# Kernel tuning notes

Measured on AMD Instinct MI355X. Metric: run time of the kernel, lower is better.

Reference implementation:

```python
import jax, jax.numpy as jnp
import numpy as np


def setup_inputs() -> dict:
    key = jax.random.key(0)
    k1, k2 = jax.random.split(key)
    D = 32            # num_detectors
    IN_S = 64         # input_size per detector
    OUT_S = 64        # output_size per detector
    B = 8192          # batch
    x = jax.random.normal(k1, (B, IN_S * D), dtype=jnp.float32)
    # nn.Linear weight: [out_features, in_features] = [OUT_S*D, IN_S*D]
    W = jax.random.normal(k2, (OUT_S * D, IN_S * D), dtype=jnp.float32) * (1.0 / np.sqrt(IN_S * D))
    return {"x": x, "W": W, "num_detectors": D}


def reference(x, W, num_detectors):
    # Original: y = ((W * block_diag_mask) @ x.T).T
    # The mask zeroes everything except num_detectors diagonal (out_s, in_s)
    # blocks, so this is exactly num_detectors independent linears. We compute
    # only the diagonal blocks (same math; off-diagonal weights contribute 0).
    D = num_detectors
    total_out, total_in = W.shape
    out_s = total_out // D
    in_s = total_in // D
    # extract diagonal blocks -> [D, out_s, in_s]
    Wb = W.reshape(D, out_s, D, in_s)
    d = jnp.arange(D)
    blocks = Wb[d, :, d, :]                      # [D, out_s, in_s]
    xb = x.reshape(x.shape[0], D, in_s)          # [B, D, in_s]
    y = jnp.einsum('bdi,doi->bdo', xb, blocks)   # [B, D, out_s]
    return y.reshape(x.shape[0], D * out_s)
```

## Files before the change

### kernel.cpp

```cpp
#include <hip/hip_runtime.h>

#define NDET    32
#define SEG     64
#define ROWLEN  2048
#define TILE_B  128
#define THREADS 256
#define LSTRIDE 72

typedef __bf16 bf16x8 __attribute__((ext_vector_type(8)));
typedef __bf16 bf16x4 __attribute__((ext_vector_type(4)));
typedef float  f32x4  __attribute__((ext_vector_type(4)));

__device__ __forceinline__ bf16x4 cvt4(f32x4 a) {
  bf16x4 r;
  r[0] = (__bf16)a[0]; r[1] = (__bf16)a[1]; r[2] = (__bf16)a[2]; r[3] = (__bf16)a[3];
  return r;
}

__global__ __launch_bounds__(THREADS) void ensemble_linear_v4(
    const float* __restrict__ x, const float* __restrict__ W,
    float* __restrict__ y) {
  const int d     = blockIdx.y;
  const int b0    = blockIdx.x * TILE_B;
  const int t     = threadIdx.x;
  const int lane  = t & 63;
  const int wid   = t >> 6;
  const int dbase = d * SEG;

  const int rq  = lane >> 4;
  const int c4  = lane & 15;

  __shared__ __bf16 wls[SEG * LSTRIDE];
  __shared__ __bf16 xls[TILE_B * LSTRIDE];

  f32x4 wv[4];
#pragma unroll
  for (int p = 0; p < 4; ++p) {
    const int row = wid * 16 + p * 4 + rq;
    wv[p] = *(const f32x4*)(W + (size_t)(dbase + row) * ROWLEN + dbase + c4 * 4);
  }
  f32x4 xv[8];
#pragma unroll
  for (int p = 0; p < 8; ++p) {
    const int row = wid * 32 + p * 4 + rq;
    xv[p] = *(const f32x4*)(x + (size_t)(b0 + row) * ROWLEN + dbase + c4 * 4);
  }

#pragma unroll
  for (int p = 0; p < 4; ++p) {
    const int row = wid * 16 + p * 4 + rq;
    *(bf16x4*)(&wls[row * LSTRIDE + c4 * 4]) = cvt4(wv[p]);
  }
#pragma unroll
  for (int p = 0; p < 8; ++p) {
    const int row = wid * 32 + p * 4 + rq;
    *(bf16x4*)(&xls[row * LSTRIDE + c4 * 4]) = cvt4(xv[p]);
  }

  __syncthreads();

  const int m16 = lane & 15;
  const int kg  = lane >> 4;

  bf16x8 wfrag[4][2];
#pragma unroll
  for (int g = 0; g < 4; ++g)
#pragma unroll
    for (int kh = 0; kh < 2; ++kh)
      wfrag[g][kh] = *(const bf16x8*)(&wls[(g * 16 + m16) * LSTRIDE + kh * 32 + kg * 8]);

#pragma unroll
  for (int s = 0; s < 2; ++s) {
    const int rbase = wid * 32 + s * 16;
    bf16x8 a0 = *(const bf16x8*)(&xls[(rbase + m16) * LSTRIDE + kg * 8]);
    bf16x8 a1 = *(const bf16x8*)(&xls[(rbase + m16) * LSTRIDE + 32 + kg * 8]);

    float* yp = y + (size_t)(b0 + rbase + m16) * ROWLEN + dbase + kg * 4;
#pragma unroll
    for (int g = 0; g < 4; ++g) {
      f32x4 acc = (f32x4){0.f, 0.f, 0.f, 0.f};
      acc = __builtin_amdgcn_mfma_f32_16x16x32_bf16(wfrag[g][0], a0, acc, 0, 0, 0);
      acc = __builtin_amdgcn_mfma_f32_16x16x32_bf16(wfrag[g][1], a1, acc, 0, 0, 0);
      *(f32x4*)(yp + g * 16) = acc;
    }
  }
}

extern "C" void kernel_launch(void* const* d_in, const int* in_sizes, int n_in,
                              void* d_out, int out_size, void* d_ws, size_t ws_size,
                              hipStream_t stream) {
  const float* x = (const float*)d_in[0];
  const float* W = (const float*)d_in[1];
  float* y = (float*)d_out;
  const int B = in_sizes[0] / ROWLEN;
  dim3 grid(B / TILE_B, NDET);
  ensemble_linear_v4<<<grid, dim3(THREADS), 0, stream>>>(x, W, y);
}
```

Measured before the change: 28.46 us.

## Tile over groups of four detectors with 64-row batch tiles

Each block now handles 64 batch rows across four adjacent detectors instead of 128 rows of one detector. The x loads read 1 KB of contiguous row data per wavefront rather than 256-byte segments, aiming at better coalescing and fewer blocks. The trade-off is that each block loads four weight blocks (64 KB fp32) for only 64 rows, so W traffic per output rises. LDS use and register pressure also grow (16+16 f32x4 staged per thread), which may lower occupancy.

```diff
diff --git a/kernel.cpp b/kernel.cpp
--- a/kernel.cpp
+++ b/kernel.cpp
@@ -3,9 +3,12 @@
 #define NDET    32
 #define SEG     64
 #define ROWLEN  2048
-#define TILE_B  128
+#define DGRP    4
+#define XCOLS   (DGRP * SEG)
+#define TILE_R  64
 #define THREADS 256
-#define LSTRIDE 72
+#define XLSTR   264
+#define WLSTR   72
 
 typedef __bf16 bf16x8 __attribute__((ext_vector_type(8)));
 typedef __bf16 bf16x4 __attribute__((ext_vector_type(4)));
@@ -17,70 +20,65 @@
   return r;
 }
 
-__global__ __launch_bounds__(THREADS) void ensemble_linear_v4(
+__global__ __launch_bounds__(THREADS) void ensemble_linear_v8(
     const float* __restrict__ x, const float* __restrict__ W,
     float* __restrict__ y) {
-  const int d     = blockIdx.y;
-  const int b0    = blockIdx.x * TILE_B;
-  const int t     = threadIdx.x;
-  const int lane  = t & 63;
-  const int wid   = t >> 6;
-  const int dbase = d * SEG;
-
+  const int dg     = blockIdx.y;
+  const int dbase0 = dg * XCOLS;
+  const int r0     = blockIdx.x * TILE_R;
+  const int t      = threadIdx.x;
+  const int lane   = t & 63;
+  const int wid    = t >> 6;
   const int rq  = lane >> 4;
   const int c4  = lane & 15;
+  const int m16 = lane & 15;
+  const int kg  = lane >> 4;
 
-  __shared__ __bf16 wls[SEG * LSTRIDE];
-  __shared__ __bf16 xls[TILE_B * LSTRIDE];
+  __shared__ __bf16 xls[TILE_R * XLSTR];
+  __shared__ __bf16 wls[DGRP * SEG * WLSTR];
 
-  f32x4 wv[4];
+  f32x4 xv[16];
 #pragma unroll
-  for (int p = 0; p < 4; ++p) {
-    const int row = wid * 16 + p * 4 + rq;
-    wv[p] = *(const f32x4*)(W + (size_t)(dbase + row) * ROWLEN + dbase + c4 * 4);
+  for (int p = 0; p < 16; ++p) {
+    const int row = p * 4 + wid;
+    xv[p] = *(const f32x4*)(x + (size_t)(r0 + row) * ROWLEN + dbase0 + lane * 4);
   }
-  f32x4 xv[8];
+
+  f32x4 wv[16];
 #pragma unroll
-  for (int p = 0; p < 8; ++p) {
-    const int row = wid * 32 + p * 4 + rq;
-    xv[p] = *(const f32x4*)(x + (size_t)(b0 + row) * ROWLEN + dbase + c4 * 4);
+  for (int p = 0; p < 16; ++p) {
+    const int o = p * 4 + rq;
+    wv[p] = *(const f32x4*)(W + (size_t)(dbase0 + wid * SEG + o) * ROWLEN
+                              + dbase0 + wid * SEG + c4 * 4);
   }
 
 #pragma unroll
-  for (int p = 0; p < 4; ++p) {
-    const int row = wid * 16 + p * 4 + rq;
-    *(bf16x4*)(&wls[row * LSTRIDE + c4 * 4]) = cvt4(wv[p]);
+  for (int p = 0; p < 16; ++p) {
+    const int row = p * 4 + wid;
+    *(bf16x4*)(&xls[row * XLSTR + lane * 4]) = cvt4(xv[p]);
   }
 #pragma unroll
-  for (int p = 0; p < 8; ++p) {
-    const int row = wid * 32 + p * 4 + rq;
-    *(bf16x4*)(&xls[row * LSTRIDE + c4 * 4]) = cvt4(xv[p]);
+  for (int p = 0; p < 16; ++p) {
+    const int o = p * 4 + rq;
+    *(bf16x4*)(&wls[(wid * SEG + o) * WLSTR + c4 * 4]) = cvt4(wv[p]);
   }
 
   __syncthreads();
 
-  const int m16 = lane & 15;
-  const int kg  = lane >> 4;
+  const int rbase = wid * 16;
+#pragma unroll
+  for (int q = 0; q < DGRP; ++q) {
+    bf16x8 a0 = *(const bf16x8*)(&xls[(rbase + m16) * XLSTR + q * SEG + kg * 8]);
+    bf16x8 a1 = *(const bf16x8*)(&xls[(rbase + m16) * XLSTR + q * SEG + 32 + kg * 8]);
 
-  bf16x8 wfrag[4][2];
-#pragma unroll
-  for (int g = 0; g < 4; ++g)
-#pragma unroll
-    for (int kh = 0; kh < 2; ++kh)
-      wfrag[g][kh] = *(const bf16x8*)(&wls[(g * 16 + m16) * LSTRIDE + kh * 32 + kg * 8]);
-
-#pragma unroll
-  for (int s = 0; s < 2; ++s) {
-    const int rbase = wid * 32 + s * 16;
-    bf16x8 a0 = *(const bf16x8*)(&xls[(rbase + m16) * LSTRIDE + kg * 8]);
-    bf16x8 a1 = *(const bf16x8*)(&xls[(rbase + m16) * LSTRIDE + 32 + kg * 8]);
-
-    float* yp = y + (size_t)(b0 + rbase + m16) * ROWLEN + dbase + kg * 4;
+    float* yp = y + (size_t)(r0 + rbase + m16) * ROWLEN + dbase0 + q * SEG + kg * 4;
 #pragma unroll
     for (int g = 0; g < 4; ++g) {
+      bf16x8 w0 = *(const bf16x8*)(&wls[(q * SEG + g * 16 + m16) * WLSTR + kg * 8]);
+      bf16x8 w1 = *(const bf16x8*)(&wls[(q * SEG + g * 16 + m16) * WLSTR + 32 + kg * 8]);
       f32x4 acc = (f32x4){0.f, 0.f, 0.f, 0.f};
-      acc = __builtin_amdgcn_mfma_f32_16x16x32_bf16(wfrag[g][0], a0, acc, 0, 0, 0);
-      acc = __builtin_amdgcn_mfma_f32_16x16x32_bf16(wfrag[g][1], a1, acc, 0, 0, 0);
+      acc = __builtin_amdgcn_mfma_f32_16x16x32_bf16(w0, a0, acc, 0, 0, 0);
+      acc = __builtin_amdgcn_mfma_f32_16x16x32_bf16(w1, a1, acc, 0, 0, 0);
       *(f32x4*)(yp + g * 16) = acc;
     }
   }
@@ -93,6 +91,6 @@
   const float* W = (const float*)d_in[1];
   float* y = (float*)d_out;
   const int B = in_sizes[0] / ROWLEN;
-  dim3 grid(B / TILE_B, NDET);
-  ensemble_linear_v4<<<grid, dim3(THREADS), 0, stream>>>(x, W, y);
+  dim3 grid(B / TILE_R, NDET / DGRP);
+  ensemble_linear_v8<<<grid, dim3(THREADS), 0, stream>>>(x, W, y);
 }
```

New measurement: 29.56 us. 1.04x slower.
